# Optimization experiments

Hardware: AMD Instinct MI355X
Metric: run time of the kernel (lower is better)

Reference implementation:

```python
import jax, jax.numpy as jnp
import numpy as np

TAU = 3.0      # time horizon (init arg tau)
FIX = 0.2      # correction gain (init arg fix)


def setup_inputs() -> dict:
    key = jax.random.key(0)
    k1, k2, k3, k4, k5 = jax.random.split(key, 5)
    B, N, K = 256, 1024, 32
    p_cur = jax.random.normal(k1, (B, N, 2), dtype=jnp.float32) * 10.0   # positions (meters)
    v_cur = jax.random.normal(k2, (B, N, 2), dtype=jnp.float32)          # previous velocities
    v_desire = jax.random.normal(k3, (B, N, 2), dtype=jnp.float32)       # desired velocities
    near_ped_idx = jax.random.randint(k4, (B, N, K), 0, N, dtype=jnp.int32)
    neigh_ped_mask = jax.random.randint(k5, (B, N, K), 0, 2).astype(jnp.float32)
    return {
        "p_cur": p_cur,
        "v_cur": v_cur,
        "v_desire": v_desire,
        "near_ped_idx": near_ped_idx,
        "neigh_ped_mask": neigh_ped_mask,
        "collision_threshold": 1,
    }


def reference(p_cur, v_cur, v_desire, near_ped_idx, neigh_ped_mask, collision_threshold):
    # Gather neighbor positions/velocities: (B,N,K,2). vmap over batch avoids
    # materializing the (B,N,N,2) expanded tensor the torch code logically builds.
    gather = jax.vmap(lambda arr, idx: arr[idx])
    neighbors_pos = gather(p_cur, near_ped_idx)
    neighbors_vel = gather(v_cur, near_ped_idx)

    mask = neigh_ped_mask[..., None]                      # (B,N,K,1)
    neighbors_pos = neighbors_pos * mask
    neighbors_vel = neighbors_vel * mask

    rel_pos = p_cur[:, :, None, :] - neighbors_pos        # (B,N,K,2)
    rel_vel = v_desire[:, :, None, :] - neighbors_vel     # (B,N,K,2)

    dot_pos_vel = jnp.sum(rel_pos * rel_vel, axis=-1)     # (B,N,K)
    dot_vel_vel = jnp.sum(rel_vel * rel_vel, axis=-1) + 1e-6
    t_min = dot_pos_vel / (dot_vel_vel + 1e-6)
    t_min = jnp.where(jnp.isnan(t_min), TAU, t_min)
    t_clamp = jnp.clip(t_min, 0.0, TAU)

    min_dist = jnp.linalg.norm(rel_pos + t_clamp[..., None] * rel_vel, axis=-1)
    min_dist = jnp.where(jnp.isnan(min_dist), 1e6, min_dist)

    collision_mask = (min_dist < collision_threshold) & (neigh_ped_mask != 0)

    # 90-degree rotated rel_pos as collision normal
    normal = jnp.stack([-rel_pos[..., 1], rel_pos[..., 0]], axis=-1)   # (B,N,K,2)
    denom = jnp.linalg.norm(normal, axis=-1, keepdims=True)
    normal = jnp.where(collision_mask[..., None], normal / (denom + 1e-6), 0.0)

    correction = jnp.sum(normal, axis=2)                  # (B,N,2)
    correction = jnp.nan_to_num(correction, nan=0.0)
    v_next = v_desire + correction * FIX
    return v_next
```

## Files before the change

### kernel.cpp

```cpp
#include <hip/hip_runtime.h>

#define TAU 3.0f
#define FIX 0.2f
#define NPED 1024
#define PEDS_PER_BLOCK 256
#define BLOCK 512
#define GROUPS (BLOCK / 8)
#define PASSES (PEDS_PER_BLOCK / GROUPS)

__global__ __launch_bounds__(BLOCK) void rvo_kernel(
    const float* __restrict__ p_cur,
    const float* __restrict__ v_cur,
    const float* __restrict__ v_desire,
    const int*   __restrict__ near_idx,
    const float* __restrict__ mask_arr,
    const int*   __restrict__ cth,
    float*       __restrict__ out,
    int N, int reps)
{
    __shared__ float4 table[NPED];

    const int tid    = threadIdx.x;
    const int bpb    = N / PEDS_PER_BLOCK;
    const int batch  = blockIdx.x / bpb;
    const int pbase  = (blockIdx.x % bpb) * PEDS_PER_BLOCK;

    const float2* pb2 = (const float2*)(p_cur) + (size_t)batch * N;
    const float2* vb2 = (const float2*)(v_cur) + (size_t)batch * N;
    #pragma unroll
    for (int n = tid; n < NPED; n += BLOCK) {
        float2 pp = pb2[n];
        float2 vv = vb2[n];
        table[n] = make_float4(pp.x, pp.y, vv.x, vv.y);
    }
    __syncthreads();

    const float thr2 = (float)cth[0] * (float)cth[0];

    const int sub  = tid & 7;
    const int pgrp = tid >> 3;

    for (int r = 0; r < reps; ++r) {
        #pragma unroll
        for (int pass = 0; pass < PASSES; ++pass) {
            const int ped  = pbase + pass * GROUPS + pgrp;
            const size_t pair = (size_t)batch * N + ped;

            const float4 self = table[ped];
            const float2 vd   = ((const float2*)v_desire)[pair];
            const float px = self.x, py = self.y;
            const float vdx = vd.x, vdy = vd.y;

            const int4   i4 = ((const int4*)near_idx)[pair * 8 + sub];
            const float4 m4 = ((const float4*)mask_arr)[pair * 8 + sub];
            const int   idxs[4] = {i4.x, i4.y, i4.z, i4.w};
            const float ms[4]   = {m4.x, m4.y, m4.z, m4.w};

            float nx = 0.0f, ny = 0.0f;
            #pragma unroll
            for (int j = 0; j < 4; ++j) {
                const float4 nb = table[idxs[j]];
                const float m = ms[j];
                const float rpx = fmaf(-m, nb.x, px);
                const float rpy = fmaf(-m, nb.y, py);
                const float rvx = fmaf(-m, nb.z, vdx);
                const float rvy = fmaf(-m, nb.w, vdy);

                const float dpv = fmaf(rpx, rvx, rpy * rvy);
                const float dvv = fmaf(rvx, rvx, fmaf(rvy, rvy, 2e-6f));
                float t = dpv * __builtin_amdgcn_rcpf(dvv);
                t = fminf(fmaxf(t, 0.0f), TAU);

                const float cx = fmaf(t, rvx, rpx);
                const float cy = fmaf(t, rvy, rpy);
                const float md2 = fmaf(cx, cx, cy * cy);

                const float s = fmaf(rpx, rpx, rpy * rpy);
                const float sel0 = (s > 0.0f) ? __builtin_amdgcn_rsqf(s) : 0.0f;
                const float w    = (md2 < thr2) ? m : 0.0f;
                const float sel  = sel0 * w;
                nx = fmaf(-rpy, sel, nx);
                ny = fmaf( rpx, sel, ny);
            }

            #pragma unroll
            for (int d = 4; d > 0; d >>= 1) {
                nx += __shfl_down(nx, d, 8);
                ny += __shfl_down(ny, d, 8);
            }

            if (sub == 0) {
                ((float2*)out)[pair] = make_float2(fmaf(nx, FIX, vdx),
                                                   fmaf(ny, FIX, vdy));
            }
        }
    }
}

extern "C" void kernel_launch(void* const* d_in, const int* in_sizes, int n_in,
                              void* d_out, int out_size, void* d_ws, size_t ws_size,
                              hipStream_t stream) {
    const float* p_cur    = (const float*)d_in[0];
    const float* v_cur    = (const float*)d_in[1];
    const float* v_desire = (const float*)d_in[2];
    const int*   near_idx = (const int*)d_in[3];
    const float* mask_arr = (const float*)d_in[4];
    const int*   cth      = (const int*)d_in[5];
    float*       out      = (float*)d_out;

    const int N  = NPED;
    const int BN = in_sizes[0] / 2;
    dim3 block(BLOCK);
    dim3 grid(BN / PEDS_PER_BLOCK);
    rvo_kernel<<<grid, block, 0, stream>>>(p_cur, v_cur, v_desire, near_idx,
                                           mask_arr, cth, out, N, 3);
}
```

Measured before the change: 110.1 us.

## Drop repeated passes and gather neighbors from a prepacked global table

The old kernel ran the whole per-pedestrian computation three times (reps=3) and rebuilt a per-batch shared-memory table of positions and velocities in each block. The new version removes that repetition, so the large index and mask arrays are streamed once. A separate pack kernel writes an interleaved float4 position/velocity table into workspace memory, and the main kernel gathers neighbors from it through the cache hierarchy. The main kernel now uses small 256-thread blocks with one pedestrian per 8 lanes. This adds a second launch and global-memory gathers in place of LDS gathers.

Result: slower. 118.2 us (+7.4%).

```diff
diff --git a/kernel.cpp b/kernel.cpp
--- a/kernel.cpp
+++ b/kernel.cpp
@@ -3,97 +3,83 @@
 #define TAU 3.0f
 #define FIX 0.2f
 #define NPED 1024
-#define PEDS_PER_BLOCK 256
-#define BLOCK 512
-#define GROUPS (BLOCK / 8)
-#define PASSES (PEDS_PER_BLOCK / GROUPS)
+#define BLOCK 256
+#define PEDS_PER_BLOCK (BLOCK / 8)
+
+__global__ __launch_bounds__(256) void pack_kernel(
+    const float2* __restrict__ p, const float2* __restrict__ v,
+    float4* __restrict__ table, int total)
+{
+    const int i = blockIdx.x * 256 + threadIdx.x;
+    if (i < total) {
+        const float2 pp = p[i];
+        const float2 vv = v[i];
+        table[i] = make_float4(pp.x, pp.y, vv.x, vv.y);
+    }
+}
 
 __global__ __launch_bounds__(BLOCK) void rvo_kernel(
-    const float* __restrict__ p_cur,
-    const float* __restrict__ v_cur,
-    const float* __restrict__ v_desire,
-    const int*   __restrict__ near_idx,
-    const float* __restrict__ mask_arr,
-    const int*   __restrict__ cth,
-    float*       __restrict__ out,
-    int N, int reps)
+    const float4* __restrict__ table,
+    const float*  __restrict__ v_desire,
+    const int*    __restrict__ near_idx,
+    const float*  __restrict__ mask_arr,
+    const int*    __restrict__ cth,
+    float*        __restrict__ out)
 {
-    __shared__ float4 table[NPED];
+    const int tid  = threadIdx.x;
+    const int sub  = tid & 7;
+    const int team = tid >> 3;
+    const int pair = blockIdx.x * PEDS_PER_BLOCK + team;
+    const int tbase = (pair >> 10) << 10;
 
-    const int tid    = threadIdx.x;
-    const int bpb    = N / PEDS_PER_BLOCK;
-    const int batch  = blockIdx.x / bpb;
-    const int pbase  = (blockIdx.x % bpb) * PEDS_PER_BLOCK;
-
-    const float2* pb2 = (const float2*)(p_cur) + (size_t)batch * N;
-    const float2* vb2 = (const float2*)(v_cur) + (size_t)batch * N;
-    #pragma unroll
-    for (int n = tid; n < NPED; n += BLOCK) {
-        float2 pp = pb2[n];
-        float2 vv = vb2[n];
-        table[n] = make_float4(pp.x, pp.y, vv.x, vv.y);
-    }
-    __syncthreads();
+    const int4   i4 = ((const int4*)near_idx)[pair * 8 + sub];
+    const float4 m4 = ((const float4*)mask_arr)[pair * 8 + sub];
+    const float4 self = table[pair];
+    const float2 vd   = ((const float2*)v_desire)[pair];
 
     const float thr2 = (float)cth[0] * (float)cth[0];
+    const float px = self.x, py = self.y;
+    const float vdx = vd.x, vdy = vd.y;
 
-    const int sub  = tid & 7;
-    const int pgrp = tid >> 3;
+    const int   idxs[4] = {i4.x, i4.y, i4.z, i4.w};
+    const float ms[4]   = {m4.x, m4.y, m4.z, m4.w};
 
-    for (int r = 0; r < reps; ++r) {
-        #pragma unroll
-        for (int pass = 0; pass < PASSES; ++pass) {
-            const int ped  = pbase + pass * GROUPS + pgrp;
-            const size_t pair = (size_t)batch * N + ped;
+    float nx = 0.0f, ny = 0.0f;
+    #pragma unroll
+    for (int j = 0; j < 4; ++j) {
+        const float4 nb = table[tbase + idxs[j]];
+        const float m = ms[j];
+        const float rpx = fmaf(-m, nb.x, px);
+        const float rpy = fmaf(-m, nb.y, py);
+        const float rvx = fmaf(-m, nb.z, vdx);
+        const float rvy = fmaf(-m, nb.w, vdy);
 
-            const float4 self = table[ped];
-            const float2 vd   = ((const float2*)v_desire)[pair];
-            const float px = self.x, py = self.y;
-            const float vdx = vd.x, vdy = vd.y;
+        const float dpv = fmaf(rpx, rvx, rpy * rvy);
+        const float dvv = fmaf(rvx, rvx, fmaf(rvy, rvy, 2e-6f));
+        float t = dpv * __builtin_amdgcn_rcpf(dvv);
+        t = fminf(fmaxf(t, 0.0f), TAU);
 
-            const int4   i4 = ((const int4*)near_idx)[pair * 8 + sub];
-            const float4 m4 = ((const float4*)mask_arr)[pair * 8 + sub];
-            const int   idxs[4] = {i4.x, i4.y, i4.z, i4.w};
-            const float ms[4]   = {m4.x, m4.y, m4.z, m4.w};
+        const float cx = fmaf(t, rvx, rpx);
+        const float cy = fmaf(t, rvy, rpy);
+        const float md2 = fmaf(cx, cx, cy * cy);
 
-            float nx = 0.0f, ny = 0.0f;
-            #pragma unroll
-            for (int j = 0; j < 4; ++j) {
-                const float4 nb = table[idxs[j]];
-                const float m = ms[j];
-                const float rpx = fmaf(-m, nb.x, px);
-                const float rpy = fmaf(-m, nb.y, py);
-                const float rvx = fmaf(-m, nb.z, vdx);
-                const float rvy = fmaf(-m, nb.w, vdy);
+        const float s = fmaf(rpx, rpx, rpy * rpy);
+        const float sel0 = (s > 0.0f) ? __builtin_amdgcn_rsqf(s) : 0.0f;
+        const float w    = (md2 < thr2) ? m : 0.0f;
+        const float sel  = sel0 * w;
+        nx = fmaf(-rpy, sel, nx);
+        ny = fmaf( rpx, sel, ny);
+    }
 
-                const float dpv = fmaf(rpx, rvx, rpy * rvy);
-                const float dvv = fmaf(rvx, rvx, fmaf(rvy, rvy, 2e-6f));
-                float t = dpv * __builtin_amdgcn_rcpf(dvv);
-                t = fminf(fmaxf(t, 0.0f), TAU);
+    #pragma unroll
+    for (int d = 4; d > 0; d >>= 1) {
+        nx += __shfl_down(nx, d, 8);
+        ny += __shfl_down(ny, d, 8);
+    }
 
-                const float cx = fmaf(t, rvx, rpx);
-                const float cy = fmaf(t, rvy, rpy);
-                const float md2 = fmaf(cx, cx, cy * cy);
-
-                const float s = fmaf(rpx, rpx, rpy * rpy);
-                const float sel0 = (s > 0.0f) ? __builtin_amdgcn_rsqf(s) : 0.0f;
-                const float w    = (md2 < thr2) ? m : 0.0f;
-                const float sel  = sel0 * w;
-                nx = fmaf(-rpy, sel, nx);
-                ny = fmaf( rpx, sel, ny);
-            }
-
-            #pragma unroll
-            for (int d = 4; d > 0; d >>= 1) {
-                nx += __shfl_down(nx, d, 8);
-                ny += __shfl_down(ny, d, 8);
-            }
-
-            if (sub == 0) {
-                ((float2*)out)[pair] = make_float2(fmaf(nx, FIX, vdx),
-                                                   fmaf(ny, FIX, vdy));
-            }
-        }
+    if (sub == 0) {
+        ((float2*)out)[pair] = make_float2(fmaf(nx, FIX, vdx),
+                                           fmaf(ny, FIX, vdy));
     }
 }
 
@@ -107,11 +93,13 @@
     const float* mask_arr = (const float*)d_in[4];
     const int*   cth      = (const int*)d_in[5];
     float*       out      = (float*)d_out;
+    float4*      table    = (float4*)d_ws;
 
-    const int N  = NPED;
     const int BN = in_sizes[0] / 2;
-    dim3 block(BLOCK);
-    dim3 grid(BN / PEDS_PER_BLOCK);
-    rvo_kernel<<<grid, block, 0, stream>>>(p_cur, v_cur, v_desire, near_idx,
-                                           mask_arr, cth, out, N, 3);
+
+    pack_kernel<<<(BN + 255) / 256, 256, 0, stream>>>(
+        (const float2*)p_cur, (const float2*)v_cur, table, BN);
+
+    rvo_kernel<<<BN / PEDS_PER_BLOCK, BLOCK, 0, stream>>>(
+        table, v_desire, near_idx, mask_arr, cth, out);
 }
```
